# Optimization experiments

Measured on AMD Instinct MI355X. Metric: run time of the kernel, lower is better.

Reference implementation:

```python
import jax, jax.numpy as jnp
import numpy as np

S, B, D, H, V = 1024, 4, 1024, 4096, 32000
EPS = 1e-5

def _ln(x, g, b):
    m = jnp.mean(x, axis=-1, keepdims=True)
    v = jnp.var(x, axis=-1, keepdims=True)
    return (x - m) * jax.lax.rsqrt(v + EPS) * g + b

def setup_inputs() -> dict:
    key = jax.random.key(0)
    ks = jax.random.split(key, 12)
    def xav(k, shape):
        fan_in, fan_out = shape[1], shape[0]
        lim = np.sqrt(6.0 / (fan_in + fan_out))
        return jax.random.uniform(k, shape, jnp.float32, -lim, lim)
    return {
        "inputs": jax.random.randint(ks[0], (S, B), 0, V, dtype=jnp.int32),
        "emb_table": jax.random.normal(ks[1], (V, D), jnp.float32),
        "WQ": xav(ks[2], (D, D)),
        "WK": xav(ks[3], (D, D)),
        "WV": xav(ks[4], (D, D)),
        "Wo": xav(ks[5], (D, D)),
        "bo": jnp.zeros((D,), jnp.float32),
        "W1": xav(ks[6], (H, D)),
        "b1": jnp.zeros((H,), jnp.float32),
        "W2": xav(ks[7], (D, H)),
        "b2": jnp.zeros((D,), jnp.float32),
        "g1": jnp.ones((D,), jnp.float32),
        "be1": jnp.zeros((D,), jnp.float32),
        "g2": jnp.ones((D,), jnp.float32),
        "be2": jnp.zeros((D,), jnp.float32),
        "Wd": xav(ks[8], (V, D)),
        "bd": jnp.zeros((V,), jnp.float32),
    }

def reference(inputs, emb_table, WQ, WK, WV, Wo, bo, W1, b1, W2, b2, g1, be1, g2, be2, Wd, bd):
    # inputs: [S, B] int ids
    emb = emb_table[inputs]                       # [S, B, D]
    # F.linear(x, W) == x @ W.T
    Q = jnp.einsum('sbd,ed->bse', emb, WQ)        # [B, S, D]
    K = jnp.einsum('sbd,ed->bse', emb, WK)
    Vv = jnp.einsum('sbd,ed->bse', emb, WV)
    scores = jnp.einsum('bqd,bkd->bqk', Q, K) / jnp.sqrt(jnp.float32(D))
    attn = jax.nn.softmax(scores, axis=-1)        # [B, S, S]
    z = jnp.einsum('bqk,bkd->qbd', attn, Vv)      # back to [S, B, D]
    z = jnp.einsum('sbd,ed->sbe', z, Wo) + bo
    x = _ln(emb + z, g1, be1)
    ffn = jnp.einsum('sbh,dh->sbd', jax.nn.relu(jnp.einsum('sbd,hd->sbh', x, W1) + b1), W2) + b2
    out = _ln(x + ffn, g2, be2)
    logits = out.reshape(S * B, D) @ Wd.T + bd    # [S*B, V]
    return logits
```

## Files before the change

### kernel.cpp

```cpp
#include <hip/hip_runtime.h>

typedef float f32x4 __attribute__((ext_vector_type(4)));
typedef __bf16 bf16x8 __attribute__((ext_vector_type(8)));
typedef int i32x4 __attribute__((ext_vector_type(4)));
typedef unsigned short u16;
typedef unsigned short u16x4 __attribute__((ext_vector_type(4)));
typedef unsigned short u16x8 __attribute__((ext_vector_type(8)));
typedef unsigned int u32;

#define SEQ 1024
#define NBATCH 4
#define DM 1024
#define HD 4096
#define NV 32000
#define NT (SEQ * NBATCH)

__device__ __forceinline__ u16 f2bf(float f) {
  u32 u = __builtin_bit_cast(u32, f);
  return (u16)((u + 0x7FFFu + ((u >> 16) & 1u)) >> 16);
}
__device__ __forceinline__ float bf2f(u16 h) {
  return __builtin_bit_cast(float, (u32)h << 16);
}

__global__ __launch_bounds__(256) void cast_all_kernel(
    const float* __restrict__ wq, const float* __restrict__ wk,
    const float* __restrict__ wv, const float* __restrict__ wo,
    const float* __restrict__ w1,
    u16* __restrict__ wqk, u16* __restrict__ wvh, u16* __restrict__ woh,
    u16* __restrict__ w1h) {
  long i = (long)blockIdx.x * 256 + threadIdx.x;
  const float* src;
  u16* dst;
  long off;
  if (i < 262144) {
    if (i < 131072) { src = wq; off = i; } else { src = wk; off = i - 131072; }
    dst = wqk + i * 8;
  } else if (i < 393216) {
    src = wv; off = i - 262144; dst = wvh + off * 8;
  } else if (i < 524288) {
    src = wo; off = i - 393216; dst = woh + off * 8;
  } else {
    src = w1; off = i - 524288; dst = w1h + off * 8;
  }
  const f32x4* p = (const f32x4*)(src + off * 8);
  f32x4 a = p[0], b = p[1];
  u16x8 o;
  o[0] = f2bf(a[0]); o[1] = f2bf(a[1]); o[2] = f2bf(a[2]); o[3] = f2bf(a[3]);
  o[4] = f2bf(b[0]); o[5] = f2bf(b[1]); o[6] = f2bf(b[2]); o[7] = f2bf(b[3]);
  *(u16x8*)dst = o;
}

__global__ __launch_bounds__(256) void embed_kernel(const int* __restrict__ ids,
                                                    const float* __restrict__ tab,
                                                    float* __restrict__ ef,
                                                    u16* __restrict__ eh) {
  int t = blockIdx.x, tid = threadIdx.x;
  long id = ids[t];
  f32x4 v = *(const f32x4*)(tab + id * DM + tid * 4);
  *(f32x4*)(ef + (long)t * DM + tid * 4) = v;
  u16x4 h;
  h[0] = f2bf(v[0]); h[1] = f2bf(v[1]); h[2] = f2bf(v[2]); h[3] = f2bf(v[3]);
  *(u16x4*)(eh + (long)t * DM + tid * 4) = h;
}

__global__ __launch_bounds__(256) void softmax_kernel(const float* __restrict__ s,
                                                      u16* __restrict__ p) {
  int row = blockIdx.x, tid = threadIdx.x;
  const float* rp = s + (long)row * SEQ;
  f32x4 v = *(const f32x4*)(rp + tid * 4);
  float mx = fmaxf(fmaxf(v[0], v[1]), fmaxf(v[2], v[3]));
  for (int o = 32; o; o >>= 1) mx = fmaxf(mx, __shfl_xor(mx, o));
  __shared__ float red[4];
  if ((tid & 63) == 0) red[tid >> 6] = mx;
  __syncthreads();
  mx = fmaxf(fmaxf(red[0], red[1]), fmaxf(red[2], red[3]));
  const float sc = 0.03125f;
  f32x4 e;
  e[0] = expf((v[0] - mx) * sc); e[1] = expf((v[1] - mx) * sc);
  e[2] = expf((v[2] - mx) * sc); e[3] = expf((v[3] - mx) * sc);
  float sm = e[0] + e[1] + e[2] + e[3];
  for (int o = 32; o; o >>= 1) sm += __shfl_xor(sm, o);
  __syncthreads();
  if ((tid & 63) == 0) red[tid >> 6] = sm;
  __syncthreads();
  sm = red[0] + red[1] + red[2] + red[3];
  float inv = 1.0f / sm;
  u16x4 o4;
  o4[0] = f2bf(e[0] * inv); o4[1] = f2bf(e[1] * inv);
  o4[2] = f2bf(e[2] * inv); o4[3] = f2bf(e[3] * inv);
  *(u16x4*)(p + (long)row * SEQ + tid * 4) = o4;
}

__global__ __launch_bounds__(256) void ln_kernel(const float* __restrict__ in,
                                                 const float* __restrict__ g,
                                                 const float* __restrict__ be,
                                                 float* __restrict__ outf,
                                                 u16* __restrict__ outh) {
  int row = blockIdx.x, tid = threadIdx.x;
  f32x4 v = *(const f32x4*)(in + (long)row * DM + tid * 4);
  float s = v[0] + v[1] + v[2] + v[3];
  float q = v[0] * v[0] + v[1] * v[1] + v[2] * v[2] + v[3] * v[3];
  for (int o = 32; o; o >>= 1) { s += __shfl_xor(s, o); q += __shfl_xor(q, o); }
  __shared__ float rs_[4], rq_[4];
  if ((tid & 63) == 0) { rs_[tid >> 6] = s; rq_[tid >> 6] = q; }
  __syncthreads();
  s = rs_[0] + rs_[1] + rs_[2] + rs_[3];
  q = rq_[0] + rq_[1] + rq_[2] + rq_[3];
  float mean = s * (1.0f / DM);
  float var = q * (1.0f / DM) - mean * mean;
  float rstd = rsqrtf(var + 1e-5f);
  f32x4 gg = *(const f32x4*)(g + tid * 4);
  f32x4 bb = *(const f32x4*)(be + tid * 4);
  f32x4 y;
  y[0] = (v[0] - mean) * rstd * gg[0] + bb[0];
  y[1] = (v[1] - mean) * rstd * gg[1] + bb[1];
  y[2] = (v[2] - mean) * rstd * gg[2] + bb[2];
  y[3] = (v[3] - mean) * rstd * gg[3] + bb[3];
  if (outf) *(f32x4*)(outf + (long)row * DM + tid * 4) = y;
  if (outh) {
    u16x4 h;
    h[0] = f2bf(y[0]); h[1] = f2bf(y[1]); h[2] = f2bf(y[2]); h[3] = f2bf(y[3]);
    *(u16x4*)(outh + (long)row * DM + tid * 4) = h;
  }
}

__global__ __launch_bounds__(256) void ln_i8_kernel(const float* __restrict__ in,
                                                    const float* __restrict__ g,
                                                    const float* __restrict__ be,
                                                    char* __restrict__ q8,
                                                    float* __restrict__ scale) {
  int row = blockIdx.x, tid = threadIdx.x;
  f32x4 v = *(const f32x4*)(in + (long)row * DM + tid * 4);
  float s = v[0] + v[1] + v[2] + v[3];
  float q = v[0] * v[0] + v[1] * v[1] + v[2] * v[2] + v[3] * v[3];
  for (int o = 32; o; o >>= 1) { s += __shfl_xor(s, o); q += __shfl_xor(q, o); }
  __shared__ float rs_[4], rq_[4], rm_[4];
  if ((tid & 63) == 0) { rs_[tid >> 6] = s; rq_[tid >> 6] = q; }
  __syncthreads();
  s = rs_[0] + rs_[1] + rs_[2] + rs_[3];
  q = rq_[0] + rq_[1] + rq_[2] + rq_[3];
  float mean = s * (1.0f / DM);
  float var = q * (1.0f / DM) - mean * mean;
  float rstd = rsqrtf(var + 1e-5f);
  f32x4 gg = *(const f32x4*)(g + tid * 4);
  f32x4 bb = *(const f32x4*)(be + tid * 4);
  f32x4 y;
  y[0] = (v[0] - mean) * rstd * gg[0] + bb[0];
  y[1] = (v[1] - mean) * rstd * gg[1] + bb[1];
  y[2] = (v[2] - mean) * rstd * gg[2] + bb[2];
  y[3] = (v[3] - mean) * rstd * gg[3] + bb[3];
  float am = fmaxf(fmaxf(fabsf(y[0]), fabsf(y[1])), fmaxf(fabsf(y[2]), fabsf(y[3])));
  for (int o = 32; o; o >>= 1) am = fmaxf(am, __shfl_xor(am, o));
  __syncthreads();
  if ((tid & 63) == 0) rm_[tid >> 6] = am;
  __syncthreads();
  am = fmaxf(fmaxf(rm_[0], rm_[1]), fmaxf(rm_[2], rm_[3]));
  float inv = (am > 0.f) ? 127.f / am : 0.f;
  int q0 = (int)rintf(y[0] * inv), q1 = (int)rintf(y[1] * inv);
  int q2 = (int)rintf(y[2] * inv), q3 = (int)rintf(y[3] * inv);
  u32 pk = (q0 & 255) | ((q1 & 255) << 8) | ((q2 & 255) << 16) | ((u32)(q3 & 255) << 24);
  *(u32*)(q8 + (size_t)row * DM + tid * 4) = pk;
  if (tid == 0) scale[row] = am * (1.0f / 127.f);
}

__global__ __launch_bounds__(256) void rowq_f32(const float* __restrict__ in,
                                                char* __restrict__ q8,
                                                float* __restrict__ scale, int rowlen) {
  const int row = blockIdx.x, tid = threadIdx.x;
  const float* rp = in + (size_t)row * rowlen;
  const int nch = rowlen >> 10;
  f32x4 v0 = {}, v1 = {}, v2 = {}, v3 = {};
  v0 = *(const f32x4*)(rp + tid * 4);
  if (nch > 1) v1 = *(const f32x4*)(rp + 1024 + tid * 4);
  if (nch > 2) v2 = *(const f32x4*)(rp + 2048 + tid * 4);
  if (nch > 3) v3 = *(const f32x4*)(rp + 3072 + tid * 4);
  auto am4 = [](f32x4 v) {
    return fmaxf(fmaxf(fabsf(v[0]), fabsf(v[1])), fmaxf(fabsf(v[2]), fabsf(v[3])));
  };
  float am = fmaxf(fmaxf(am4(v0), am4(v1)), fmaxf(am4(v2), am4(v3)));
  for (int o = 32; o; o >>= 1) am = fmaxf(am, __shfl_xor(am, o));
  __shared__ float rm_[4];
  if ((tid & 63) == 0) rm_[tid >> 6] = am;
  __syncthreads();
  am = fmaxf(fmaxf(rm_[0], rm_[1]), fmaxf(rm_[2], rm_[3]));
  const float inv = (am > 0.f) ? 127.f / am : 0.f;
  auto pack = [&](f32x4 v) {
    int q0 = (int)rintf(v[0] * inv), q1 = (int)rintf(v[1] * inv);
    int q2 = (int)rintf(v[2] * inv), q3 = (int)rintf(v[3] * inv);
    return (u32)((q0 & 255) | ((q1 & 255) << 8) | ((q2 & 255) << 16) | ((u32)(q3 & 255) << 24));
  };
  char* qp = q8 + (size_t)row * rowlen;
  *(u32*)(qp + tid * 4) = pack(v0);
  if (nch > 1) *(u32*)(qp + 1024 + tid * 4) = pack(v1);
  if (nch > 2) *(u32*)(qp + 2048 + tid * 4) = pack(v2);
  if (nch > 3) *(u32*)(qp + 3072 + tid * 4) = pack(v3);
  if (tid == 0) scale[row] = am * (1.0f / 127.f);
}

__global__ __launch_bounds__(256) void rowq_bf16_hd(const u16* __restrict__ in,
                                                    char* __restrict__ q8,
                                                    float* __restrict__ scale) {
  const int row = blockIdx.x, tid = threadIdx.x;
  const u16* rp = in + (size_t)row * HD;
  f32x4 v0, v1, v2, v3;
  auto ld4 = [&](int off) {
    u16x4 h = *(const u16x4*)(rp + off + tid * 4);
    f32x4 v;
    v[0] = bf2f(h[0]); v[1] = bf2f(h[1]); v[2] = bf2f(h[2]); v[3] = bf2f(h[3]);
    return v;
  };
  v0 = ld4(0); v1 = ld4(1024); v2 = ld4(2048); v3 = ld4(3072);
  auto am4 = [](f32x4 v) {
    return fmaxf(fmaxf(fabsf(v[0]), fabsf(v[1])), fmaxf(fabsf(v[2]), fabsf(v[3])));
  };
  float am = fmaxf(fmaxf(am4(v0), am4(v1)), fmaxf(am4(v2), am4(v3)));
  for (int o = 32; o; o >>= 1) am = fmaxf(am, __shfl_xor(am, o));
  __shared__ float rm_[4];
  if ((tid & 63) == 0) rm_[tid >> 6] = am;
  __syncthreads();
  am = fmaxf(fmaxf(rm_[0], rm_[1]), fmaxf(rm_[2], rm_[3]));
  const float inv = (am > 0.f) ? 127.f / am : 0.f;
  auto pack = [&](f32x4 v) {
    int q0 = (int)rintf(v[0] * inv), q1 = (int)rintf(v[1] * inv);
    int q2 = (int)rintf(v[2] * inv), q3 = (int)rintf(v[3] * inv);
    return (u32)((q0 & 255) | ((q1 & 255) << 8) | ((q2 & 255) << 16) | ((u32)(q3 & 255) << 24));
  };
  char* qp = q8 + (size_t)row * HD;
  *(u32*)(qp + tid * 4) = pack(v0);
  *(u32*)(qp + 1024 + tid * 4) = pack(v1);
  *(u32*)(qp + 2048 + tid * 4) = pack(v2);
  *(u32*)(qp + 3072 + tid * 4) = pack(v3);
  if (tid == 0) scale[row] = am * (1.0f / 127.f);
}

#define GLD(gp, lp)                                              \
  __builtin_amdgcn_global_load_lds(                              \
      (__attribute__((address_space(1))) void*)(gp),             \
      (__attribute__((address_space(3))) void*)(lp), 16, 0, 0)

#define BM 128
#define BN 128
#define BK 32

__global__ __launch_bounds__(256) void gemm_bt(
    const u16* __restrict__ A, const u16* __restrict__ B,
    float* __restrict__ Cf, u16* __restrict__ Ch,
    const float* __restrict__ bias, const float* __restrict__ resid,
    int K, int lda, int ldb, int ldc,
    long batA, long batB, long batC, int relu) {
  __shared__ u16 As[BM * BK];
  __shared__ u16 Bs[BN * BK];
  const int tid = threadIdx.x;
  const int bz = blockIdx.z;
  A += (long)bz * batA;
  B += (long)bz * batB;
  const long cbase = (long)bz * batC;
  const int row0 = blockIdx.y * BM;
  const int col0 = blockIdx.x * BN;
  const int l = tid & 63;
  const int w = tid >> 6;
  const int wr = (w >> 1) * 64, wc = (w & 1) * 64;

  f32x4 acc[4][4] = {};

  const u16* gA = A + (long)(row0 + (tid >> 2)) * lda + (tid & 3) * 8;
  const u16* gB = B + (long)(col0 + (tid >> 2)) * ldb + (tid & 3) * 8;
  const long a64 = (long)64 * lda, b64 = (long)64 * ldb;
  u16* lA = As + tid * 8;
  u16* lB = Bs + tid * 8;

  const int fr = l & 15;
  const int fk = (l >> 4) * 8;
  const u16* rA = As + (wr + fr) * BK + fk;
  const u16* rB = Bs + (wc + fr) * BK + fk;

  for (int k0 = 0; k0 < K; k0 += BK) {
    GLD(gA + k0, lA);
    GLD(gA + a64 + k0, lA + 2048);
    GLD(gB + k0, lB);
    GLD(gB + b64 + k0, lB + 2048);
    __syncthreads();
    bf16x8 af[4], bf[4];
#pragma unroll
    for (int m = 0; m < 4; ++m) af[m] = *(const bf16x8*)(rA + m * 16 * BK);
#pragma unroll
    for (int n = 0; n < 4; ++n) bf[n] = *(const bf16x8*)(rB + n * 16 * BK);
#pragma unroll
    for (int m = 0; m < 4; ++m)
#pragma unroll
      for (int n = 0; n < 4; ++n)
        acc[m][n] = __builtin_amdgcn_mfma_f32_16x16x32_bf16(af[m], bf[n], acc[m][n], 0, 0, 0);
    __syncthreads();
  }

  const int er = row0 + wr + ((l >> 4) << 2);
  const int ec = col0 + wc + (l & 15);
#pragma unroll
  for (int m = 0; m < 4; ++m) {
#pragma unroll
    for (int n = 0; n < 4; ++n) {
      f32x4 v = acc[m][n];
      const int c = ec + n * 16;
      float bv = bias ? bias[c] : 0.0f;
#pragma unroll
      for (int i = 0; i < 4; ++i) {
        const int r = er + m * 16 + i;
        float x = v[i] + bv;
        if (resid) x += resid[(long)r * ldc + c];
        if (relu) x = fmaxf(x, 0.0f);
        if (Cf) Cf[cbase + (long)r * ldc + c] = x;
        if (Ch) Ch[cbase + (long)r * ldc + c] = f2bf(x);
      }
    }
  }
}

#define DSB() __builtin_amdgcn_sched_barrier(0)
#define SBAR() __builtin_amdgcn_s_barrier()

__global__ __launch_bounds__(256) void gemm_i8(
    const char* __restrict__ A, const char* __restrict__ B,
    float* __restrict__ C, const float* __restrict__ sA, const float* __restrict__ sB,
    const float* __restrict__ bias, const float* __restrict__ resid,
    int K, int lda, int ldb, int ldc, int Mtiles, int Ntiles) {
  __shared__ __align__(16) char As[3][128 * 64];
  __shared__ __align__(16) char Bs[3][128 * 64];
  const int tid = threadIdx.x;

  const int nwg = gridDim.x;
  const int blk = blockIdx.x;
  const int cpx = nwg >> 3;
  const int wg = (blk & 7) * cpx + (blk >> 3);
  const int row0 = (wg / Ntiles) * 128;
  const int col0 = (wg % Ntiles) * 128;

  const int l = tid & 63;
  const int w = tid >> 6;
  const int wr = (w >> 1) * 64, wc = (w & 1) * 64;

  const int srow = tid >> 2;
  const int sslot = (tid & 3) ^ ((srow >> 1) & 3);
  const char* gA = A + (size_t)(row0 + srow) * lda + sslot * 16;
  const char* gB = B + (size_t)(col0 + srow) * ldb + sslot * 16;
  const size_t a64 = (size_t)64 * lda, b64 = (size_t)64 * ldb;

#define STAGE_I8(buf, kt)                                            \
  do {                                                               \
    const char* _ga = gA + (size_t)(kt) * 64;                        \
    const char* _gb = gB + (size_t)(kt) * 64;                        \
    GLD(_ga, &As[buf][0] + tid * 16);                                \
    GLD(_ga + a64, &As[buf][4096] + tid * 16);                       \
    GLD(_gb, &Bs[buf][0] + tid * 16);                                \
    GLD(_gb + b64, &Bs[buf][4096] + tid * 16);                       \
  } while (0)

  const int fr = l & 15;
  const int fsw = 16 * ((l >> 4) ^ ((fr >> 1) & 3));
  const int raoff = (wr + fr) * 64 + fsw;
  const int rboff = (wc + fr) * 64 + fsw;

  i32x4 acc[4][4] = {};

#define COMPUTE_I8(buf)                                                         \
  do {                                                                          \
    i32x4 af[4], bf[4];                                                         \
    _Pragma("unroll")                                                           \
    for (int m = 0; m < 4; ++m) af[m] = *(const i32x4*)(&As[buf][raoff + m * 1024]); \
    _Pragma("unroll")                                                           \
    for (int n = 0; n < 4; ++n) bf[n] = *(const i32x4*)(&Bs[buf][rboff + n * 1024]); \
    _Pragma("unroll")                                                           \
    for (int m = 0; m < 4; ++m)                                                 \
      _Pragma("unroll")                                                         \
      for (int n = 0; n < 4; ++n)                                               \
        acc[m][n] = __builtin_amdgcn_mfma_i32_16x16x64_i8(af[m], bf[n], acc[m][n], 0, 0, 0); \
  } while (0)

#define PIPE_STEP(bufS, kt, bufC)                    \
  do {                                               \
    STAGE_I8(bufS, kt);                              \
    COMPUTE_I8(bufC);                                \
    asm volatile("s_waitcnt vmcnt(4)"); DSB();       \
    SBAR();                                          \
  } while (0)

  const int nkt = K >> 6;

  STAGE_I8(0, 0);
  STAGE_I8(1, 1);
  asm volatile("s_waitcnt vmcnt(4)"); DSB();
  SBAR();

  for (int t = 0; t + 7 <= nkt; t += 3) {
    PIPE_STEP(2, t + 2, 0);
    PIPE_STEP(0, t + 3, 1);
    PIPE_STEP(1, t + 4, 2);
  }
  PIPE_STEP(2, nkt - 2, 0);
  PIPE_STEP(0, nkt - 1, 1);
  COMPUTE_I8(2);
  asm volatile("s_waitcnt vmcnt(0)"); DSB();
  SBAR();
  COMPUTE_I8(0);

  const int er = row0 + wr + ((l >> 4) << 2);
  const int ec = col0 + wc + (l & 15);
#pragma unroll
  for (int m = 0; m < 4; ++m) {
#pragma unroll
    for (int n = 0; n < 4; ++n) {
      i32x4 v = acc[m][n];
      const int c = ec + n * 16;
      const float sb = sB[c];
      const float bv = bias ? bias[c] : 0.0f;
#pragma unroll
      for (int i = 0; i < 4; ++i) {
        const int r = er + m * 16 + i;
        float x = (float)v[i] * (sA[r] * sb) + bv;
        if (resid) x += resid[(size_t)r * ldc + c];
        C[(size_t)r * ldc + c] = x;
      }
    }
  }
#undef STAGE_I8
#undef COMPUTE_I8
#undef PIPE_STEP
}

__global__ __launch_bounds__(256) void gemm_i8_m256(
    const char* __restrict__ A, const char* __restrict__ B,
    float* __restrict__ C, const float* __restrict__ sA, const float* __restrict__ sB,
    const float* __restrict__ bias, int K, int lda, int ldb, int ldc,
    int Mtiles, int Ntiles) {
  __shared__ __align__(16) char As[3][256 * 64];
  __shared__ __align__(16) char Bs[3][128 * 64];
  const int tid = threadIdx.x;

  const int nwg = gridDim.x;
  const int blk = blockIdx.x;
  const int cpx = nwg >> 3;
  const int wg = (blk & 7) * cpx + (blk >> 3);
  const int row0 = (wg / Ntiles) * 256;
  const int col0 = (wg % Ntiles) * 128;

  const int l = tid & 63;
  const int w = tid >> 6;
  const int wr = (w >> 1) * 128, wc = (w & 1) * 64;

  const int srow = tid >> 2;
  const int sslot = (tid & 3) ^ ((srow >> 1) & 3);
  const char* gA = A + (size_t)(row0 + srow) * lda + sslot * 16;
  const char* gB = B + (size_t)(col0 + srow) * ldb + sslot * 16;
  const size_t a64 = (size_t)64 * lda, b64 = (size_t)64 * ldb;

#define STAGE_M256(buf, kt)                                          \
  do {                                                               \
    const char* _ga = gA + (size_t)(kt) * 64;                        \
    const char* _gb = gB + (size_t)(kt) * 64;                        \
    GLD(_ga, &As[buf][0] + tid * 16);                                \
    GLD(_ga + a64, &As[buf][4096] + tid * 16);                       \
    GLD(_ga + 2 * a64, &As[buf][8192] + tid * 16);                   \
    GLD(_ga + 3 * a64, &As[buf][12288] + tid * 16);                  \
    GLD(_gb, &Bs[buf][0] + tid * 16);                                \
    GLD(_gb + b64, &Bs[buf][4096] + tid * 16);                       \
  } while (0)

  const int fr = l & 15;
  const int fsw = 16 * ((l >> 4) ^ ((fr >> 1) & 3));
  const int raoff = (wr + fr) * 64 + fsw;
  const int rboff = (wc + fr) * 64 + fsw;

  i32x4 acc[8][4] = {};

#define COMPUTE_M256(buf)                                                       \
  do {                                                                          \
    i32x4 af[8], bf[4];                                                         \
    _Pragma("unroll")                                                           \
    for (int m = 0; m < 8; ++m) af[m] = *(const i32x4*)(&As[buf][raoff + m * 1024]); \
    _Pragma("unroll")                                                           \
    for (int n = 0; n < 4; ++n) bf[n] = *(const i32x4*)(&Bs[buf][rboff + n * 1024]); \
    _Pragma("unroll")                                                           \
    for (int m = 0; m < 8; ++m)                                                 \
      _Pragma("unroll")                                                         \
      for (int n = 0; n < 4; ++n)                                               \
        acc[m][n] = __builtin_amdgcn_mfma_i32_16x16x64_i8(af[m], bf[n], acc[m][n], 0, 0, 0); \
  } while (0)

#define PIPE_M256(bufS, kt, bufC)                    \
  do {                                               \
    STAGE_M256(bufS, kt);                            \
    COMPUTE_M256(bufC);                              \
    asm volatile("s_waitcnt vmcnt(6)"); DSB();       \
    SBAR();                                          \
  } while (0)

  const int nkt = K >> 6;

  STAGE_M256(0, 0);
  STAGE_M256(1, 1);
  asm volatile("s_waitcnt vmcnt(6)"); DSB();
  SBAR();

  for (int t = 0; t + 7 <= nkt; t += 3) {
    PIPE_M256(2, t + 2, 0);
    PIPE_M256(0, t + 3, 1);
    PIPE_M256(1, t + 4, 2);
  }
  PIPE_M256(2, nkt - 2, 0);
  PIPE_M256(0, nkt - 1, 1);
  COMPUTE_M256(2);
  asm volatile("s_waitcnt vmcnt(0)"); DSB();
  SBAR();
  COMPUTE_M256(0);

  const int er = row0 + wr + ((l >> 4) << 2);
  const int ec = col0 + wc + (l & 15);
#pragma unroll
  for (int m = 0; m < 8; ++m) {
#pragma unroll
    for (int n = 0; n < 4; ++n) {
      i32x4 v = acc[m][n];
      const int c = ec + n * 16;
      const float sb = sB[c];
      const float bv = bias ? bias[c] : 0.0f;
#pragma unroll
      for (int i = 0; i < 4; ++i) {
        const int r = er + m * 16 + i;
        C[(size_t)r * ldc + c] = (float)v[i] * (sA[r] * sb) + bv;
      }
    }
  }
#undef STAGE_M256
#undef COMPUTE_M256
#undef PIPE_M256
}

template <int N0, int N1>
__device__ __forceinline__ void mfma16(f32x4 (&acc)[8][4], const bf16x8 (&af)[8],
                                       bf16x8 b0, bf16x8 b1) {
#pragma unroll
  for (int m = 0; m < 8; ++m) {
    acc[m][N0] = __builtin_amdgcn_mfma_f32_16x16x32_bf16(af[m], b0, acc[m][N0], 0, 0, 0);
    acc[m][N1] = __builtin_amdgcn_mfma_f32_16x16x32_bf16(af[m], b1, acc[m][N1], 0, 0, 0);
  }
}

__global__ __launch_bounds__(512, 2) void gemm256_bt(
    const u16* __restrict__ A, const u16* __restrict__ B,
    float* __restrict__ Cf, u16* __restrict__ Ch,
    const float* __restrict__ bias,
    int K, int lda, int ldb, int ldc, int Mtiles, int Ntiles, int relu) {
  __shared__ __align__(16) u16 As[2][2][128 * 64];
  __shared__ __align__(16) u16 Bs[2][2][256 * 32];
  const int tid = threadIdx.x;

  const int nwg = gridDim.x;
  const int blk = blockIdx.x;
  const int cpx = nwg >> 3;
  const int wg = (blk & 7) * cpx + (blk >> 3);
  const int gsz = 4 * Ntiles;
  const int gid = wg / gsz;
  const int rem = wg - gid * gsz;
  const int row0 = (gid * 4 + (rem & 3)) * 256;
  const int col0 = (rem >> 2) * 256;

  const int l = tid & 63;
  const int w = tid >> 6;
  const int wr = w >> 2;
  const int wc = w & 3;

  const int sArow = tid >> 3;
  const int sAcol = ((tid & 7) ^ ((sArow >> 1) & 7)) * 8;
  const int sBrow = tid >> 2;
  const int sBcol = ((tid & 3) ^ ((sBrow >> 2) & 3)) * 8;

  const u16* gA = A + (size_t)(row0 + sArow) * lda + sAcol;
  const u16* gB = B + (size_t)(col0 + sBrow) * ldb + sBcol;
  const size_t a64 = (size_t)64 * lda;
  const size_t b128 = (size_t)128 * ldb;

#define STAGE_A(buf, h, kt)                                          \
  do {                                                               \
    const u16* _g = gA + (size_t)(h) * 128 * lda + (size_t)(kt) * 64;\
    u16* _l = &As[buf][h][0] + tid * 8;                              \
    GLD(_g, _l);                                                     \
    GLD(_g + a64, _l + 4096);                                        \
  } while (0)
#define STAGE_B(buf, kk, kt)                                         \
  do {                                                               \
    const u16* _g = gB + (size_t)(kt) * 64 + (kk) * 32;              \
    u16* _l = &Bs[buf][kk][0] + tid * 8;                             \
    GLD(_g, _l);                                                     \
    GLD(_g + b128, _l + 4096);                                       \
  } while (0)

  const int fr = l & 15;
  const int g8 = (l >> 4) * 8;
  const int acp0 = g8 ^ (((fr >> 1) & 7) * 8);
  const int acp1 = (32 + g8) ^ (((fr >> 1) & 7) * 8);
  const int bcp = g8 ^ (((fr >> 2) & 3) * 8);

#define RA(buf, m, cp) (*(const bf16x8*)(&As[buf][wr][((m) * 16 + fr) * 64 + (cp)]))
#define RB(buf, n, kk) (*(const bf16x8*)(&Bs[buf][kk][(wc * 64 + (n) * 16 + fr) * 32 + bcp]))

  f32x4 acc[8][4] = {};
  bf16x8 a0[8], a1[8], bb0, bb1;

  const int nkt = K >> 6;
  const int nit = nkt >> 1;

  STAGE_A(0, 0, 0); STAGE_A(0, 1, 0);
  STAGE_B(0, 0, 0); STAGE_B(0, 1, 0);
  STAGE_B(1, 0, 1); STAGE_A(1, 0, 1);
  asm volatile("s_waitcnt vmcnt(4)"); DSB();
  SBAR();

  for (int i = 0; i < nit; ++i) {
    const int u = 2 * i + 1;
    const int v = (2 * i + 2 < nkt) ? 2 * i + 2 : nkt - 1;
    const int w2 = (2 * i + 3 < nkt) ? 2 * i + 3 : nkt - 1;

#pragma unroll
    for (int m = 0; m < 8; ++m) a0[m] = RA(0, m, acp0);
    bb0 = RB(0, 0, 0); bb1 = RB(0, 1, 0);
    STAGE_A(1, 1, u);
    SBAR();
    asm volatile("s_waitcnt lgkmcnt(0)"); DSB();
    __builtin_amdgcn_s_setprio(1);
    mfma16<0, 1>(acc, a0, bb0, bb1);
    __builtin_amdgcn_s_setprio(0);
    SBAR();
    bb0 = RB(0, 2, 0); bb1 = RB(0, 3, 0);
    STAGE_B(1, 1, u);
    asm volatile("s_waitcnt vmcnt(6)"); DSB();
    SBAR();
    asm volatile("s_waitcnt lgkmcnt(0)"); DSB();
    __builtin_amdgcn_s_setprio(1);
    mfma16<2, 3>(acc, a0, bb0, bb1);
    __builtin_amdgcn_s_setprio(0);
    SBAR();
#pragma unroll
    for (int m = 0; m < 8; ++m) a1[m] = RA(0, m, acp1);
    bb0 = RB(0, 0, 1); bb1 = RB(0, 1, 1);
    STAGE_B(0, 0, v);
    SBAR();
    asm volatile("s_waitcnt lgkmcnt(0)"); DSB();
    __builtin_amdgcn_s_setprio(1);
    mfma16<0, 1>(acc, a1, bb0, bb1);
    __builtin_amdgcn_s_setprio(0);
    SBAR();
    bb0 = RB(0, 2, 1); bb1 = RB(0, 3, 1);
    STAGE_A(0, 0, v);
    asm volatile("s_waitcnt vmcnt(6)"); DSB();
    SBAR();
    asm volatile("s_waitcnt lgkmcnt(0)"); DSB();
    __builtin_amdgcn_s_setprio(1);
    mfma16<2, 3>(acc, a1, bb0, bb1);
    __builtin_amdgcn_s_setprio(0);
    SBAR();
#pragma unroll
    for (int m = 0; m < 8; ++m) a0[m] = RA(1, m, acp0);
    bb0 = RB(1, 0, 0); bb1 = RB(1, 1, 0);
    STAGE_A(0, 1, v);
    SBAR();
    asm volatile("s_waitcnt lgkmcnt(0)"); DSB();
    __builtin_amdgcn_s_setprio(1);
    mfma16<0, 1>(acc, a0, bb0, bb1);
    __builtin_amdgcn_s_setprio(0);
    SBAR();
    bb0 = RB(1, 2, 0); bb1 = RB(1, 3, 0);
    STAGE_B(0, 1, v);
    asm volatile("s_waitcnt vmcnt(6)"); DSB();
    SBAR();
    asm volatile("s_waitcnt lgkmcnt(0)"); DSB();
    __builtin_amdgcn_s_setprio(1);
    mfma16<2, 3>(acc, a0, bb0, bb1);
    __builtin_amdgcn_s_setprio(0);
    SBAR();
#pragma unroll
    for (int m = 0; m < 8; ++m) a1[m] = RA(1, m, acp1);
    bb0 = RB(1, 0, 1); bb1 = RB(1, 1, 1);
    STAGE_B(1, 0, w2);
    SBAR();
    asm volatile("s_waitcnt lgkmcnt(0)"); DSB();
    __builtin_amdgcn_s_setprio(1);
    mfma16<0, 1>(acc, a1, bb0, bb1);
    __builtin_amdgcn_s_setprio(0);
    SBAR();
    bb0 = RB(1, 2, 1); bb1 = RB(1, 3, 1);
    STAGE_A(1, 0, w2);
    asm volatile("s_waitcnt vmcnt(6)"); DSB();
    SBAR();
    asm volatile("s_waitcnt lgkmcnt(0)"); DSB();
    __builtin_amdgcn_s_setprio(1);
    mfma16<2, 3>(acc, a1, bb0, bb1);
    __builtin_amdgcn_s_setprio(0);
    SBAR();
  }

  asm volatile("s_waitcnt vmcnt(0)"); DSB();

  const int er = row0 + wr * 128 + ((l >> 4) << 2);
  const int ec = col0 + wc * 64 + (l & 15);
#pragma unroll
  for (int m = 0; m < 8; ++m) {
#pragma unroll
    for (int n = 0; n < 4; ++n) {
      f32x4 vv = acc[m][n];
      const int c = ec + n * 16;
      float bv = bias ? bias[c] : 0.0f;
#pragma unroll
      for (int i = 0; i < 4; ++i) {
        const int r = er + m * 16 + i;
        float x = vv[i] + bv;
        if (relu) x = fmaxf(x, 0.0f);
        if (Cf) Cf[(size_t)r * ldc + c] = x;
        if (Ch) Ch[(size_t)r * ldc + c] = f2bf(x);
      }
    }
  }
#undef STAGE_A
#undef STAGE_B
#undef RA
#undef RB
}

extern "C" void kernel_launch(void* const* d_in, const int* in_sizes, int n_in,
                              void* d_out, int out_size, void* d_ws, size_t ws_size,
                              hipStream_t stream) {
  const int* ids = (const int*)d_in[0];
  const float* tab = (const float*)d_in[1];
  const float* WQ = (const float*)d_in[2];
  const float* WK = (const float*)d_in[3];
  const float* WV = (const float*)d_in[4];
  const float* Wo = (const float*)d_in[5];
  const float* bo = (const float*)d_in[6];
  const float* W1 = (const float*)d_in[7];
  const float* b1 = (const float*)d_in[8];
  const float* W2 = (const float*)d_in[9];
  const float* b2 = (const float*)d_in[10];
  const float* g1 = (const float*)d_in[11];
  const float* be1 = (const float*)d_in[12];
  const float* g2 = (const float*)d_in[13];
  const float* be2 = (const float*)d_in[14];
  const float* Wd = (const float*)d_in[15];
  const float* bd = (const float*)d_in[16];
  float* logits = (float*)d_out;

  if (ws_size < 280000000ull) return;

  char* p = (char*)d_ws;
  auto alloc = [&](size_t bytes) {
    char* r = p;
    p += (bytes + 255) & ~(size_t)255;
    return r;
  };
  float* embf = (float*)alloc((size_t)NT * DM * 4);
  u16* embh = (u16*)alloc((size_t)NT * DM * 2);
  u16* WQKh = (u16*)alloc((size_t)2 * DM * DM * 2);
  u16* WVh = (u16*)alloc((size_t)DM * DM * 2);
  u16* Woh = (u16*)alloc((size_t)DM * DM * 2);
  u16* W1h = (u16*)alloc((size_t)HD * DM * 2);
  char* W2q = (char*)alloc((size_t)DM * HD);
  float* sW2 = (float*)alloc((size_t)DM * 4);
  char* Wdq = (char*)alloc((size_t)NV * DM);
  float* sWd = (float*)alloc((size_t)NV * 4);
  u16* QKh = (u16*)alloc((size_t)NT * 2 * DM * 2);
  u16* VTh = (u16*)alloc((size_t)NBATCH * DM * SEQ * 2);
  float* scoresf = (float*)alloc((size_t)NBATCH * SEQ * SEQ * 4);
  u16* Ph = (u16*)alloc((size_t)NBATCH * SEQ * SEQ * 2);
  u16* zh = (u16*)alloc((size_t)NT * DM * 2);
  float* r1f = (float*)alloc((size_t)NT * DM * 4);
  float* xf = (float*)alloc((size_t)NT * DM * 4);
  u16* xh = (u16*)alloc((size_t)NT * DM * 2);
  u16* hh = (u16*)alloc((size_t)NT * HD * 2);
  char* hq = (char*)alloc((size_t)NT * HD);
  float* sH = (float*)alloc((size_t)NT * 4);
  float* r2f = (float*)alloc((size_t)NT * DM * 4);
  char* outq = (char*)alloc((size_t)NT * DM);
  float* sOut = (float*)alloc((size_t)NT * 4);

  cast_all_kernel<<<dim3(4096), 256, 0, stream>>>(WQ, WK, WV, Wo, W1,
                                                  WQKh, WVh, Woh, W1h);
  rowq_f32<<<dim3(NV), 256, 0, stream>>>(Wd, Wdq, sWd, DM);
  rowq_f32<<<dim3(DM), 256, 0, stream>>>(W2, W2q, sW2, HD);

  embed_kernel<<<NT, 256, 0, stream>>>(ids, tab, embf, embh);

  gemm_bt<<<dim3(2 * DM / BN, NT / BM, 1), 256, 0, stream>>>(
      embh, WQKh, nullptr, QKh, nullptr, nullptr, DM, DM, DM, 2 * DM, 0, 0, 0, 0);

  gemm_bt<<<dim3(SEQ / BN, DM / BM, NBATCH), 256, 0, stream>>>(
      WVh, embh, nullptr, VTh, nullptr, nullptr, DM, DM, NBATCH * DM, SEQ,
      0, DM, (long)DM * SEQ, 0);

  gemm_bt<<<dim3(SEQ / BN, SEQ / BM, NBATCH), 256, 0, stream>>>(
      QKh, QKh + DM, scoresf, nullptr, nullptr, nullptr, DM,
      NBATCH * 2 * DM, NBATCH * 2 * DM, SEQ,
      2 * DM, 2 * DM, (long)SEQ * SEQ, 0);

  softmax_kernel<<<NBATCH * SEQ, 256, 0, stream>>>(scoresf, Ph);

  gemm_bt<<<dim3(DM / BN, SEQ / BM, NBATCH), 256, 0, stream>>>(
      Ph, VTh, nullptr, zh, nullptr, nullptr, SEQ, SEQ, SEQ, NBATCH * DM,
      (long)SEQ * SEQ, (long)DM * SEQ, DM, 0);

  gemm_bt<<<dim3(DM / BN, NT / BM, 1), 256, 0, stream>>>(
      zh, Woh, r1f, nullptr, bo, embf, DM, DM, DM, DM, 0, 0, 0, 0);

  ln_kernel<<<NT, 256, 0, stream>>>(r1f, g1, be1, xf, xh);

  gemm256_bt<<<dim3((NT / 256) * (HD / 256)), 512, 0, stream>>>(
      xh, W1h, nullptr, hh, b1, DM, DM, DM, HD, NT / 256, HD / 256, 1);

  rowq_bf16_hd<<<dim3(NT), 256, 0, stream>>>(hh, hq, sH);

  gemm_i8<<<dim3((NT / 128) * (DM / 128)), 256, 0, stream>>>(
      hq, W2q, r2f, sH, sW2, b2, xf, HD, HD, HD, DM, NT / 128, DM / 128);

  ln_i8_kernel<<<NT, 256, 0, stream>>>(r2f, g2, be2, outq, sOut);

  gemm_i8_m256<<<dim3((NT / 256) * (NV / 128)), 256, 0, stream>>>(
      outq, Wdq, logits, sOut, sWd, bd, DM, DM, DM, NV, NT / 256, NV / 128);
}
```

Baseline: 725.2 us.

## Use 128x128 tiles with XCD-sliced column mapping for logits GEMM

The int8 vocabulary-projection GEMM moves from 256x128 tiles to 128x128 tiles. The vocabulary dimension is padded to 32768 so the column tiles split evenly across the 8 XCDs. Each XCD now owns a contiguous slice of vocabulary columns and iterates over all row tiles, so its slice of the quantized Wd can stay resident in that XCD's L2. The trade-offs are doubled A-tile reloads, lower per-wave MFMA reuse, wasted compute on padded columns, and reads of uninitialized padded weight rows whose results are masked before the store.

```diff
diff --git a/kernel.cpp b/kernel.cpp
--- a/kernel.cpp
+++ b/kernel.cpp
@@ -13,6 +13,7 @@
 #define DM 1024
 #define HD 4096
 #define NV 32000
+#define NVP 32768
 #define NT (SEQ * NBATCH)
 
 __device__ __forceinline__ u16 f2bf(float f) {
@@ -427,25 +428,27 @@
 #undef PIPE_STEP
 }
 
-__global__ __launch_bounds__(256) void gemm_i8_m256(
+__global__ __launch_bounds__(256) void gemm_i8_ns(
     const char* __restrict__ A, const char* __restrict__ B,
     float* __restrict__ C, const float* __restrict__ sA, const float* __restrict__ sB,
     const float* __restrict__ bias, int K, int lda, int ldb, int ldc,
-    int Mtiles, int Ntiles) {
-  __shared__ __align__(16) char As[3][256 * 64];
+    int Mtiles, int Ntiles, int validN) {
+  __shared__ __align__(16) char As[3][128 * 64];
   __shared__ __align__(16) char Bs[3][128 * 64];
   const int tid = threadIdx.x;
 
-  const int nwg = gridDim.x;
   const int blk = blockIdx.x;
-  const int cpx = nwg >> 3;
-  const int wg = (blk & 7) * cpx + (blk >> 3);
-  const int row0 = (wg / Ntiles) * 256;
-  const int col0 = (wg % Ntiles) * 128;
+  const int xcd = blk & 7;
+  const int local = blk >> 3;
+  const int nsl = Ntiles >> 3;
+  const int m = local / nsl;
+  const int nl = local - m * nsl;
+  const int row0 = m * 128;
+  const int col0 = (xcd * nsl + nl) * 128;
 
   const int l = tid & 63;
   const int w = tid >> 6;
-  const int wr = (w >> 1) * 128, wc = (w & 1) * 64;
+  const int wr = (w >> 1) * 64, wc = (w & 1) * 64;
 
   const int srow = tid >> 2;
   const int sslot = (tid & 3) ^ ((srow >> 1) & 3);
@@ -453,14 +456,12 @@
   const char* gB = B + (size_t)(col0 + srow) * ldb + sslot * 16;
   const size_t a64 = (size_t)64 * lda, b64 = (size_t)64 * ldb;
 
-#define STAGE_M256(buf, kt)                                          \
+#define STAGE_NS(buf, kt)                                            \
   do {                                                               \
     const char* _ga = gA + (size_t)(kt) * 64;                        \
     const char* _gb = gB + (size_t)(kt) * 64;                        \
     GLD(_ga, &As[buf][0] + tid * 16);                                \
     GLD(_ga + a64, &As[buf][4096] + tid * 16);                       \
-    GLD(_ga + 2 * a64, &As[buf][8192] + tid * 16);                   \
-    GLD(_ga + 3 * a64, &As[buf][12288] + tid * 16);                  \
     GLD(_gb, &Bs[buf][0] + tid * 16);                                \
     GLD(_gb + b64, &Bs[buf][4096] + tid * 16);                       \
   } while (0)
@@ -470,69 +471,70 @@
   const int raoff = (wr + fr) * 64 + fsw;
   const int rboff = (wc + fr) * 64 + fsw;
 
-  i32x4 acc[8][4] = {};
-
-#define COMPUTE_M256(buf)                                                       \
+  i32x4 acc[4][4] = {};
+
+#define COMPUTE_NS(buf)                                                         \
   do {                                                                          \
-    i32x4 af[8], bf[4];                                                         \
+    i32x4 af[4], bf[4];                                                         \
     _Pragma("unroll")                                                           \
-    for (int m = 0; m < 8; ++m) af[m] = *(const i32x4*)(&As[buf][raoff + m * 1024]); \
+    for (int m_ = 0; m_ < 4; ++m_) af[m_] = *(const i32x4*)(&As[buf][raoff + m_ * 1024]); \
     _Pragma("unroll")                                                           \
-    for (int n = 0; n < 4; ++n) bf[n] = *(const i32x4*)(&Bs[buf][rboff + n * 1024]); \
+    for (int n_ = 0; n_ < 4; ++n_) bf[n_] = *(const i32x4*)(&Bs[buf][rboff + n_ * 1024]); \
     _Pragma("unroll")                                                           \
-    for (int m = 0; m < 8; ++m)                                                 \
+    for (int m_ = 0; m_ < 4; ++m_)                                              \
       _Pragma("unroll")                                                         \
-      for (int n = 0; n < 4; ++n)                                               \
-        acc[m][n] = __builtin_amdgcn_mfma_i32_16x16x64_i8(af[m], bf[n], acc[m][n], 0, 0, 0); \
+      for (int n_ = 0; n_ < 4; ++n_)                                            \
+        acc[m_][n_] = __builtin_amdgcn_mfma_i32_16x16x64_i8(af[m_], bf[n_], acc[m_][n_], 0, 0, 0); \
   } while (0)
 
-#define PIPE_M256(bufS, kt, bufC)                    \
+#define PIPE_NS(bufS, kt, bufC)                      \
   do {                                               \
-    STAGE_M256(bufS, kt);                            \
-    COMPUTE_M256(bufC);                              \
-    asm volatile("s_waitcnt vmcnt(6)"); DSB();       \
+    STAGE_NS(bufS, kt);                              \
+    COMPUTE_NS(bufC);                                \
+    asm volatile("s_waitcnt vmcnt(4)"); DSB();       \
     SBAR();                                          \
   } while (0)
 
   const int nkt = K >> 6;
 
-  STAGE_M256(0, 0);
-  STAGE_M256(1, 1);
-  asm volatile("s_waitcnt vmcnt(6)"); DSB();
+  STAGE_NS(0, 0);
+  STAGE_NS(1, 1);
+  asm volatile("s_waitcnt vmcnt(4)"); DSB();
   SBAR();
 
   for (int t = 0; t + 7 <= nkt; t += 3) {
-    PIPE_M256(2, t + 2, 0);
-    PIPE_M256(0, t + 3, 1);
-    PIPE_M256(1, t + 4, 2);
-  }
-  PIPE_M256(2, nkt - 2, 0);
-  PIPE_M256(0, nkt - 1, 1);
-  COMPUTE_M256(2);
+    PIPE_NS(2, t + 2, 0);
+    PIPE_NS(0, t + 3, 1);
+    PIPE_NS(1, t + 4, 2);
+  }
+  PIPE_NS(2, nkt - 2, 0);
+  PIPE_NS(0, nkt - 1, 1);
+  COMPUTE_NS(2);
   asm volatile("s_waitcnt vmcnt(0)"); DSB();
   SBAR();
-  COMPUTE_M256(0);
+  COMPUTE_NS(0);
 
   const int er = row0 + wr + ((l >> 4) << 2);
   const int ec = col0 + wc + (l & 15);
 #pragma unroll
-  for (int m = 0; m < 8; ++m) {
-#pragma unroll
-    for (int n = 0; n < 4; ++n) {
-      i32x4 v = acc[m][n];
-      const int c = ec + n * 16;
+  for (int m_ = 0; m_ < 4; ++m_) {
+#pragma unroll
+    for (int n_ = 0; n_ < 4; ++n_) {
+      i32x4 v = acc[m_][n_];
+      const int c = ec + n_ * 16;
+      if (c >= validN) continue;
       const float sb = sB[c];
       const float bv = bias ? bias[c] : 0.0f;
 #pragma unroll
       for (int i = 0; i < 4; ++i) {
-        const int r = er + m * 16 + i;
+        const int r = er + m_ * 16 + i;
         C[(size_t)r * ldc + c] = (float)v[i] * (sA[r] * sb) + bv;
       }
     }
   }
-#undef STAGE_M256
-#undef COMPUTE_M256
-#undef PIPE_M256
+#undef STAGE_NS
+#undef COMPUTE_NS
+#undef PIPE_NS
 }
 
 template <int N0, int N1>
@@ -763,8 +765,8 @@
   u16* W1h = (u16*)alloc((size_t)HD * DM * 2);
   char* W2q = (char*)alloc((size_t)DM * HD);
   float* sW2 = (float*)alloc((size_t)DM * 4);
-  char* Wdq = (char*)alloc((size_t)NV * DM);
-  float* sWd = (float*)alloc((size_t)NV * 4);
+  char* Wdq = (char*)alloc((size_t)NVP * DM);
+  float* sWd = (float*)alloc((size_t)NVP * 4);
   u16* QKh = (u16*)alloc((size_t)NT * 2 * DM * 2);
   u16* VTh = (u16*)alloc((size_t)NBATCH * DM * SEQ * 2);
   float* scoresf = (float*)alloc((size_t)NBATCH * SEQ * SEQ * 4);
@@ -820,6 +822,7 @@
 
   ln_i8_kernel<<<NT, 256, 0, stream>>>(r2f, g2, be2, outq, sOut);
 
-  gemm_i8_m256<<<dim3((NT / 256) * (NV / 128)), 256, 0, stream>>>(
-      outq, Wdq, logits, sOut, sWd, bd, DM, DM, DM, NV, NT / 256, NV / 128);
-}
+  gemm_i8_ns<<<dim3((NT / 128) * (NVP / 128)), 256, 0, stream>>>(
+      outq, Wdq, logits, sOut, sWd, bd, DM, DM, DM, NV,
+      NT / 128, NVP / 128, NV);
+}
```

Result: faster. 649.6 us (-10.4%).
